# Kernel optimization log

Measured on AMD Instinct MI355X. Metric: run time of the kernel, lower is better.

The kernel has to match this reference:

```python
import jax, jax.numpy as jnp
import numpy as np

N = 100000      # nodes
E = 1600000     # edges
F_IN = 128
HID = 64
N_CLS = 40


def setup_inputs() -> dict:
    key = jax.random.key(0)
    ks = jax.random.split(key, 8)
    x = jax.random.normal(ks[0], (N, F_IN), dtype=jnp.float32)
    edge_index = jax.random.randint(ks[1], (2, E), 0, N, dtype=jnp.int64)
    # SAGEConv params: lin_l (applied to mean-aggregated neighbors, with bias),
    # lin_r (applied to root/self features, no bias). Glorot-ish init scaling.
    W1_l = jax.random.normal(ks[2], (F_IN, HID), dtype=jnp.float32) / np.sqrt(F_IN)
    b1 = jnp.zeros((HID,), dtype=jnp.float32)
    W1_r = jax.random.normal(ks[3], (F_IN, HID), dtype=jnp.float32) / np.sqrt(F_IN)
    W2_l = jax.random.normal(ks[4], (HID, N_CLS), dtype=jnp.float32) / np.sqrt(HID)
    b2 = jnp.zeros((N_CLS,), dtype=jnp.float32)
    W2_r = jax.random.normal(ks[5], (HID, N_CLS), dtype=jnp.float32) / np.sqrt(HID)
    return {"x": x, "edge_index": edge_index,
            "W1_l": W1_l, "b1": b1, "W1_r": W1_r,
            "W2_l": W2_l, "b2": b2, "W2_r": W2_r}


def _sage_conv(x, src, dst, W_l, b_l, W_r):
    # mean aggregation of neighbor features: messages flow src -> dst
    msgs = x[src]                                              # [E, d]
    summed = jax.ops.segment_sum(msgs, dst, num_segments=N)    # [N, d]
    cnt = jax.ops.segment_sum(jnp.ones((src.shape[0],), x.dtype), dst,
                              num_segments=N)                  # [N]
    agg = summed / jnp.maximum(cnt, 1.0)[:, None]
    return agg @ W_l + b_l + x @ W_r


def reference(x, edge_index, W1_l, b1, W1_r, W2_l, b2, W2_r):
    src, dst = edge_index[0], edge_index[1]
    h = jax.nn.relu(_sage_conv(x, src, dst, W1_l, b1, W1_r))
    # dropout: identity in eval mode
    logits = _sage_conv(h, src, dst, W2_l, b2, W2_r)
    return jax.nn.log_softmax(logits, axis=1)
```

## Files before the change

### kernel.cpp

```cpp
#include <hip/hip_runtime.h>
#include <math.h>

#define N_NODES 100000
#define F_IN    128
#define HID     64
#define N_CLS   40
#define MT      (N_NODES / 16)

#define BSHIFT  9
#define BSZ     512
#define NB      ((N_NODES + BSZ - 1) / BSZ)
#define EPB     4096

typedef __attribute__((ext_vector_type(8))) short bf8_t;
typedef __attribute__((ext_vector_type(4))) float f4_t;
typedef __attribute__((ext_vector_type(2))) float f2v_t;

typedef unsigned short ushort_t;
typedef unsigned int uint_t;
typedef unsigned char uchar_t;

__device__ __forceinline__ ushort_t f2b(float f) {
    union { float f; uint_t u; } c; c.f = f;
    uint_t u = c.u + 0x7FFFu + ((c.u >> 16) & 1u);
    return (ushort_t)(u >> 16);
}
__device__ __forceinline__ float b2f(ushort_t h) {
    union { uint_t u; float f; } c; c.u = ((uint_t)h) << 16;
    return c.f;
}

#if defined(__has_builtin)
#if __has_builtin(__builtin_amdgcn_cvt_pk_f32_fp8) && __has_builtin(__builtin_amdgcn_cvt_pk_fp8_f32)
#define HAVE_FP8_HW 1
#endif
#endif

__device__ __forceinline__ uchar_t fp8_enc(float v) {
#ifdef HAVE_FP8_HW
    return (uchar_t)(__builtin_amdgcn_cvt_pk_fp8_f32(v, v, 0, false) & 0xff);
#else
    union { float f; uint_t u; } c; c.f = v;
    uint_t s = c.u >> 31;
    float av = fabsf(v);
    if (av > 448.f) av = 448.f;
    int e;
    float m = frexpf(av, &e);
    int ee = e + 6;
    uchar_t r;
    if (av == 0.f) r = 0;
    else if (ee <= 0) {
        int q = (int)(av * 512.f + 0.5f);
        if (q > 7) q = 7;
        r = (uchar_t)q;
    } else {
        int q = (int)(m * 16.f + 0.5f);
        if (q == 16) { q = 8; ee += 1; }
        if (ee > 15) { ee = 15; q = 15; }
        r = (uchar_t)((ee << 3) | (q & 7));
    }
    return r | (uchar_t)(s << 7);
#endif
}

__device__ __forceinline__ f2v_t fp8x2_dec_lo(uint_t w) {
#ifdef HAVE_FP8_HW
    return __builtin_amdgcn_cvt_pk_f32_fp8(w, false);
#else
    f2v_t r;
    for (int k = 0; k < 2; ++k) {
        uchar_t b = (w >> (8 * k)) & 0xff;
        uint_t s = (b >> 7) & 1, e = (b >> 3) & 15, m = b & 7;
        float f;
        if (e) { union { uint_t u; float ff; } c;
                 c.u = (s << 31) | ((e + 120) << 23) | (m << 20); f = c.ff; }
        else   { f = (float)m * 0.001953125f; if (s) f = -f; }
        r[k] = f;
    }
    return r;
#endif
}
__device__ __forceinline__ f2v_t fp8x2_dec_hi(uint_t w) {
#ifdef HAVE_FP8_HW
    return __builtin_amdgcn_cvt_pk_f32_fp8(w, true);
#else
    return fp8x2_dec_lo(w >> 16);
#endif
}

__global__ void block_hist_kernel(const int* __restrict__ ei, int E,
                                  int* __restrict__ blockHist) {
    __shared__ int cnt[NB];
    int t = threadIdx.x, blk = blockIdx.x;
    for (int i = t; i < NB; i += 256) cnt[i] = 0;
    __syncthreads();
    int e0 = blk * EPB;
#pragma unroll
    for (int i = 0; i < EPB / 256; ++i) {
        int e = e0 + i * 256 + t;
        if (e < E) atomicAdd(&cnt[ei[E + e] >> BSHIFT], 1);
    }
    __syncthreads();
    for (int i = t; i < NB; i += 256) blockHist[blk * NB + i] = cnt[i];
}

__global__ void col_scan_kernel(const int* __restrict__ blockHist, int nblk,
                                int* __restrict__ blockBase,
                                int* __restrict__ btot) {
    __shared__ int ss[256];
    __shared__ int carry;
    int bin = blockIdx.x, t = threadIdx.x;
    if (t == 0) carry = 0;
    __syncthreads();
    for (int c0 = 0; c0 < nblk; c0 += 256) {
        int b = c0 + t;
        int v = (b < nblk) ? blockHist[b * NB + bin] : 0;
        ss[t] = v;
        __syncthreads();
        for (int off = 1; off < 256; off <<= 1) {
            int u = (t >= off) ? ss[t - off] : 0;
            __syncthreads();
            ss[t] += u;
            __syncthreads();
        }
        if (b < nblk) blockBase[b * NB + bin] = carry + ss[t] - v;
        __syncthreads();
        if (t == 255) carry += ss[255];
        __syncthreads();
    }
    if (t == 0) btot[bin] = carry;
}

__global__ void scatter_pairs_kernel(const int* __restrict__ ei, int E,
                                     const int* __restrict__ blockBase,
                                     const int* __restrict__ btot,
                                     uint_t* __restrict__ pairs) {
    __shared__ int cur[NB];
    __shared__ int base[NB];
    __shared__ int ss[256];
    int t = threadIdx.x, blk = blockIdx.x;
    int v = (t < NB) ? btot[t] : 0;
    ss[t] = v;
    __syncthreads();
    for (int off = 1; off < 256; off <<= 1) {
        int u = (t >= off) ? ss[t - off] : 0;
        __syncthreads();
        ss[t] += u;
        __syncthreads();
    }
    if (t < NB) {
        cur[t] = 0;
        base[t] = (ss[t] - v) + blockBase[blk * NB + t];
    }
    __syncthreads();
    int e0 = blk * EPB;
#pragma unroll
    for (int i = 0; i < EPB / 256; ++i) {
        int e = e0 + i * 256 + t;
        if (e < E) {
            int src = ei[e];
            int dst = ei[E + e];
            int bin = dst >> BSHIFT;
            int r = atomicAdd(&cur[bin], 1);
            pairs[base[bin] + r] = ((uint_t)src << BSHIFT) | (uint_t)(dst & (BSZ - 1));
        }
    }
}

__global__ void bucket_sort_kernel(const uint_t* __restrict__ pairs,
                                   const int* __restrict__ btot,
                                   int* __restrict__ rowptr,
                                   int* __restrict__ csr) {
    __shared__ int hist[BSZ];
    __shared__ int lofs[BSZ];
    int bin = blockIdx.x, t = threadIdx.x;
    int pv = (t < NB) ? btot[t] : 0;
    lofs[t] = pv;
    __syncthreads();
    for (int off = 1; off < BSZ; off <<= 1) {
        int u = (t >= off) ? lofs[t - off] : 0;
        __syncthreads();
        lofs[t] += u;
        __syncthreads();
    }
    int base = (bin > 0) ? lofs[bin - 1] : 0;
    int cnt = btot[bin];
    __syncthreads();
    hist[t] = 0;
    __syncthreads();
    for (int i = t; i < cnt; i += BSZ)
        atomicAdd(&hist[pairs[base + i] & (BSZ - 1)], 1);
    __syncthreads();
    int v = hist[t];
    lofs[t] = v;
    __syncthreads();
    for (int off = 1; off < BSZ; off <<= 1) {
        int u = (t >= off) ? lofs[t - off] : 0;
        __syncthreads();
        lofs[t] += u;
        __syncthreads();
    }
    int excl = lofs[t] - v;
    int d_global = (bin << BSHIFT) + t;
    if (d_global < N_NODES) rowptr[d_global] = base + excl;
    if (bin == NB - 1 && t == 0) rowptr[N_NODES] = base + cnt;
    __syncthreads();
    lofs[t] = excl;
    hist[t] = 0;
    __syncthreads();
    for (int i = t; i < cnt; i += BSZ) {
        uint_t p = pairs[base + i];
        int lb = p & (BSZ - 1);
        int r = atomicAdd(&hist[lb], 1);
        csr[base + lofs[lb] + r] = (int)(p >> BSHIFT);
    }
}

__global__ void cvt_w_kernel(const float* __restrict__ W1l,
                             const float* __restrict__ W1r,
                             const float* __restrict__ W2l,
                             const float* __restrict__ W2r,
                             ushort_t* __restrict__ W1t,
                             ushort_t* __restrict__ W2t) {
    int t = blockIdx.x * blockDim.x + threadIdx.x;
    if (t < 128 * F_IN) {
        int n = t / F_IN, k = t - n * F_IN;
        float v = (n < HID) ? W1l[k * HID + n] : W1r[k * HID + (n - HID)];
        W1t[t] = f2b(v);
    } else if (t < 128 * F_IN + 80 * HID) {
        int u = t - 128 * F_IN;
        int n = u / HID, k = u - n * HID;
        float v = (n < N_CLS) ? W2l[k * N_CLS + n] : W2r[k * N_CLS + (n - N_CLS)];
        W2t[u] = f2b(v);
    }
}

__global__ void gemm1_mfma_kernel(const float* __restrict__ x,
                                  const ushort_t* __restrict__ W1t,
                                  uchar_t* __restrict__ y1f8,
                                  ushort_t* __restrict__ z1b) {
    __shared__ uchar_t sy[128][80];
    __shared__ ushort_t sz[128][72];
    int tid = threadIdx.x;
    int wave = tid >> 6, lane = tid & 63;
    int tile0 = blockIdx.x * 8 + wave * 2;
    int m0b = blockIdx.x * 128;
    int r = lane & 15, q = lane >> 4;
    bool v0 = (tile0 < MT), v1 = (tile0 + 1 < MT);

    bf8_t a0[4], a1[4];
#pragma unroll
    for (int kt = 0; kt < 4; ++kt) { a0[kt] = (bf8_t)(short)0; a1[kt] = (bf8_t)(short)0; }
    if (v0) {
        const float* xr = x + (size_t)(tile0 * 16 + r) * F_IN + q * 8;
#pragma unroll
        for (int kt = 0; kt < 4; ++kt) {
            float4 u = *(const float4*)(xr + kt * 32);
            float4 v = *(const float4*)(xr + kt * 32 + 4);
            bf8_t tt;
            tt[0] = (short)f2b(u.x); tt[1] = (short)f2b(u.y);
            tt[2] = (short)f2b(u.z); tt[3] = (short)f2b(u.w);
            tt[4] = (short)f2b(v.x); tt[5] = (short)f2b(v.y);
            tt[6] = (short)f2b(v.z); tt[7] = (short)f2b(v.w);
            a0[kt] = tt;
        }
    }
    if (v1) {
        const float* xr = x + (size_t)((tile0 + 1) * 16 + r) * F_IN + q * 8;
#pragma unroll
        for (int kt = 0; kt < 4; ++kt) {
            float4 u = *(const float4*)(xr + kt * 32);
            float4 v = *(const float4*)(xr + kt * 32 + 4);
            bf8_t tt;
            tt[0] = (short)f2b(u.x); tt[1] = (short)f2b(u.y);
            tt[2] = (short)f2b(u.z); tt[3] = (short)f2b(u.w);
            tt[4] = (short)f2b(v.x); tt[5] = (short)f2b(v.y);
            tt[6] = (short)f2b(v.z); tt[7] = (short)f2b(v.w);
            a1[kt] = tt;
        }
    }
    int lr0 = wave * 32 + q * 4;
#pragma unroll
    for (int tn = 0; tn < 8; ++tn) {
        const ushort_t* wr = W1t + (size_t)(tn * 16 + r) * F_IN + q * 8;
        bf8_t b[4];
#pragma unroll
        for (int kt = 0; kt < 4; ++kt)
            b[kt] = *(const bf8_t*)(wr + kt * 32);
        f4_t acc0 = {0.f, 0.f, 0.f, 0.f};
        f4_t acc1 = {0.f, 0.f, 0.f, 0.f};
#pragma unroll
        for (int kt = 0; kt < 4; ++kt) {
            acc0 = __builtin_amdgcn_mfma_f32_16x16x32_bf16(a0[kt], b[kt], acc0, 0, 0, 0);
            acc1 = __builtin_amdgcn_mfma_f32_16x16x32_bf16(a1[kt], b[kt], acc1, 0, 0, 0);
        }
        int col = tn * 16 + r;
        if (col < 64) {
            if (v0) {
#pragma unroll
                for (int rr = 0; rr < 4; ++rr) sy[lr0 + rr][col] = fp8_enc(acc0[rr]);
            }
            if (v1) {
#pragma unroll
                for (int rr = 0; rr < 4; ++rr) sy[lr0 + 16 + rr][col] = fp8_enc(acc1[rr]);
            }
        } else {
            if (v0) {
#pragma unroll
                for (int rr = 0; rr < 4; ++rr) sz[lr0 + rr][col - 64] = f2b(acc0[rr]);
            }
            if (v1) {
#pragma unroll
                for (int rr = 0; rr < 4; ++rr) sz[lr0 + 16 + rr][col - 64] = f2b(acc1[rr]);
            }
        }
    }
    __syncthreads();
    int vrows = N_NODES - m0b; if (vrows > 128) vrows = 128;
    for (int idx = tid; idx < vrows * 4; idx += 256) {
        int row = idx >> 2, c = (idx & 3) << 4;
        *(uint4*)(y1f8 + (size_t)(m0b + row) * 64 + c) = *(const uint4*)&sy[row][c];
    }
    for (int idx = tid; idx < vrows * 8; idx += 256) {
        int row = idx >> 3, c = (idx & 7) << 3;
        *(uint4*)(z1b + (size_t)(m0b + row) * HID + c) = *(const uint4*)&sz[row][c];
    }
}

__device__ __forceinline__ void acc16(float* acc, uint4 v) {
    f2v_t p;
    p = fp8x2_dec_lo(v.x); acc[0]  += p[0]; acc[1]  += p[1];
    p = fp8x2_dec_hi(v.x); acc[2]  += p[0]; acc[3]  += p[1];
    p = fp8x2_dec_lo(v.y); acc[4]  += p[0]; acc[5]  += p[1];
    p = fp8x2_dec_hi(v.y); acc[6]  += p[0]; acc[7]  += p[1];
    p = fp8x2_dec_lo(v.z); acc[8]  += p[0]; acc[9]  += p[1];
    p = fp8x2_dec_hi(v.z); acc[10] += p[0]; acc[11] += p[1];
    p = fp8x2_dec_lo(v.w); acc[12] += p[0]; acc[13] += p[1];
    p = fp8x2_dec_hi(v.w); acc[14] += p[0]; acc[15] += p[1];
}

__global__ void agg1_kernel(const int* __restrict__ rowptr,
                            const int* __restrict__ csr,
                            const uchar_t* __restrict__ y1f8,
                            const ushort_t* __restrict__ z1b,
                            const float* __restrict__ b1,
                            ushort_t* __restrict__ hb,
                            uchar_t* __restrict__ hf8) {
    int gid = blockIdx.x * blockDim.x + threadIdx.x;
    int wave = gid >> 6, lane = gid & 63;
    int g = lane >> 2, l = lane & 3;
    int n = wave * 16 + g;
    if (n >= N_NODES) return;
    int beg = rowptr[n], end = rowptr[n + 1];
    float acc[16];
#pragma unroll
    for (int j = 0; j < 16; ++j) acc[j] = 0.f;
    const uchar_t* yb = y1f8 + l * 16;
    int i = beg;
    for (; i + 3 < end; i += 4) {
        int s0 = csr[i], s1 = csr[i + 1], s2 = csr[i + 2], s3 = csr[i + 3];
        uint4 w0 = *(const uint4*)(yb + (size_t)s0 * 64);
        uint4 w1 = *(const uint4*)(yb + (size_t)s1 * 64);
        uint4 w2 = *(const uint4*)(yb + (size_t)s2 * 64);
        uint4 w3 = *(const uint4*)(yb + (size_t)s3 * 64);
        acc16(acc, w0); acc16(acc, w1); acc16(acc, w2); acc16(acc, w3);
    }
    for (; i < end; ++i) {
        uint4 w = *(const uint4*)(yb + (size_t)csr[i] * 64);
        acc16(acc, w);
    }
    float inv = 1.0f / fmaxf((float)(end - beg), 1.0f);
    int c = l * 16;
    ushort_t zz[16];
    *(uint4*)&zz[0] = *(const uint4*)(z1b + (size_t)n * HID + c);
    *(uint4*)&zz[8] = *(const uint4*)(z1b + (size_t)n * HID + c + 8);
    float bv[16];
    *(float4*)&bv[0]  = *(const float4*)(b1 + c);
    *(float4*)&bv[4]  = *(const float4*)(b1 + c + 4);
    *(float4*)&bv[8]  = *(const float4*)(b1 + c + 8);
    *(float4*)&bv[12] = *(const float4*)(b1 + c + 12);
    ushort_t o[16];
    uchar_t of[16];
#pragma unroll
    for (int j = 0; j < 16; ++j) {
        float r = fmaxf(fmaf(acc[j], inv, bv[j] + b2f(zz[j])), 0.f);
        o[j] = f2b(r);
        of[j] = fp8_enc(r);
    }
    *(uint4*)(hb + (size_t)n * HID + c)     = *(const uint4*)&o[0];
    *(uint4*)(hb + (size_t)n * HID + c + 8) = *(const uint4*)&o[8];
    *(uint4*)(hf8 + (size_t)n * 64 + c)     = *(const uint4*)&of[0];
}

__global__ void agg2m_kernel(const int* __restrict__ rowptr,
                             const int* __restrict__ csr,
                             const uchar_t* __restrict__ hf8,
                             ushort_t* __restrict__ mb) {
    int gid = blockIdx.x * blockDim.x + threadIdx.x;
    int wave = gid >> 6, lane = gid & 63;
    int g = lane >> 2, l = lane & 3;
    int n = wave * 16 + g;
    if (n >= N_NODES) return;
    int beg = rowptr[n], end = rowptr[n + 1];
    float acc[16];
#pragma unroll
    for (int j = 0; j < 16; ++j) acc[j] = 0.f;
    const uchar_t* yb = hf8 + l * 16;
    int i = beg;
    for (; i + 3 < end; i += 4) {
        int s0 = csr[i], s1 = csr[i + 1], s2 = csr[i + 2], s3 = csr[i + 3];
        uint4 w0 = *(const uint4*)(yb + (size_t)s0 * 64);
        uint4 w1 = *(const uint4*)(yb + (size_t)s1 * 64);
        uint4 w2 = *(const uint4*)(yb + (size_t)s2 * 64);
        uint4 w3 = *(const uint4*)(yb + (size_t)s3 * 64);
        acc16(acc, w0); acc16(acc, w1); acc16(acc, w2); acc16(acc, w3);
    }
    for (; i < end; ++i) {
        uint4 w = *(const uint4*)(yb + (size_t)csr[i] * 64);
        acc16(acc, w);
    }
    float inv = 1.0f / fmaxf((float)(end - beg), 1.0f);
    int c = l * 16;
    ushort_t o[16];
#pragma unroll
    for (int j = 0; j < 16; ++j)
        o[j] = f2b(acc[j] * inv);
    *(uint4*)(mb + (size_t)n * HID + c)     = *(const uint4*)&o[0];
    *(uint4*)(mb + (size_t)n * HID + c + 8) = *(const uint4*)&o[8];
}

__global__ void gemm2_fused_kernel(const ushort_t* __restrict__ mb,
                                   const ushort_t* __restrict__ hb,
                                   const ushort_t* __restrict__ W2t,
                                   const float* __restrict__ b2,
                                   float* __restrict__ out) {
    __shared__ float sOut[64][44];
    int tid = threadIdx.x;
    int wave = tid >> 6, lane = tid & 63;
    int tile = blockIdx.x * 4 + wave;
    int m0b = blockIdx.x * 64;
    if (tile < MT) {
        int m0 = tile * 16;
        int r = lane & 15, q = lane >> 4;
        const ushort_t* mr = mb + (size_t)(m0 + r) * HID + q * 8;
        const ushort_t* hr = hb + (size_t)(m0 + r) * HID + q * 8;
        bf8_t a0[2], a1[2];
#pragma unroll
        for (int kt = 0; kt < 2; ++kt) {
            a0[kt] = *(const bf8_t*)(mr + kt * 32);
            a1[kt] = *(const bf8_t*)(hr + kt * 32);
        }
        float v[3][4];
#pragma unroll
        for (int tn = 0; tn < 3; ++tn) {
            int col = tn * 16 + r;
            int cl = (col < N_CLS) ? col : 0;
            const ushort_t* wl = W2t + (size_t)cl * HID + q * 8;
            const ushort_t* wrp = W2t + (size_t)(N_CLS + cl) * HID + q * 8;
            f4_t acc = {0.f, 0.f, 0.f, 0.f};
#pragma unroll
            for (int kt = 0; kt < 2; ++kt) {
                bf8_t bl = *(const bf8_t*)(wl + kt * 32);
                acc = __builtin_amdgcn_mfma_f32_16x16x32_bf16(a0[kt], bl, acc, 0, 0, 0);
            }
#pragma unroll
            for (int kt = 0; kt < 2; ++kt) {
                bf8_t br = *(const bf8_t*)(wrp + kt * 32);
                acc = __builtin_amdgcn_mfma_f32_16x16x32_bf16(a1[kt], br, acc, 0, 0, 0);
            }
            float bias = (col < N_CLS) ? b2[cl] : 0.f;
#pragma unroll
            for (int rr = 0; rr < 4; ++rr)
                v[tn][rr] = (col < N_CLS) ? (acc[rr] + bias) : -INFINITY;
        }
        int lrow = wave * 16 + q * 4;
#pragma unroll
        for (int rr = 0; rr < 4; ++rr) {
            float m = fmaxf(fmaxf(v[0][rr], v[1][rr]), v[2][rr]);
#pragma unroll
            for (int off = 1; off < 16; off <<= 1)
                m = fmaxf(m, __shfl_xor(m, off, 64));
            float s = 0.f;
#pragma unroll
            for (int tn = 0; tn < 3; ++tn)
                if (v[tn][rr] > -INFINITY) s += expf(v[tn][rr] - m);
#pragma unroll
            for (int off = 1; off < 16; off <<= 1)
                s += __shfl_xor(s, off, 64);
            float ls = m + logf(s);
#pragma unroll
            for (int tn = 0; tn < 3; ++tn) {
                int col = tn * 16 + r;
                if (col < N_CLS)
                    sOut[lrow + rr][col] = v[tn][rr] - ls;
            }
        }
    }
    __syncthreads();
    int vrows = N_NODES - m0b; if (vrows > 64) vrows = 64;
    for (int idx = tid; idx < vrows * 10; idx += 256) {
        int row = idx / 10, c = (idx - row * 10) * 4;
        *(float4*)(out + (size_t)(m0b + row) * N_CLS + c) = *(const float4*)&sOut[row][c];
    }
}

extern "C" void kernel_launch(void* const* d_in, const int* in_sizes, int n_in,
                              void* d_out, int out_size, void* d_ws, size_t ws_size,
                              hipStream_t stream) {
    const float* x   = (const float*)d_in[0];
    const int*   ei  = (const int*)d_in[1];
    const float* W1l = (const float*)d_in[2];
    const float* b1  = (const float*)d_in[3];
    const float* W1r = (const float*)d_in[4];
    const float* W2l = (const float*)d_in[5];
    const float* b2  = (const float*)d_in[6];
    const float* W2r = (const float*)d_in[7];
    float* out = (float*)d_out;
    const int E = in_sizes[1] / 2;
    const int nblk = (E + EPB - 1) / EPB;

    char* p = (char*)d_ws;
    auto take = [&](size_t bytes) {
        char* q = p;
        p += (bytes + 15) & ~(size_t)15;
        return (void*)q;
    };
    int* rowptr     = (int*)take(sizeof(int) * (N_NODES + 4));
    int* blockHist  = (int*)take(sizeof(int) * (size_t)nblk * NB);
    int* blockBase  = (int*)take(sizeof(int) * (size_t)nblk * NB);
    int* btot       = (int*)take(sizeof(int) * NB);
    uint_t* pairs   = (uint_t*)take(sizeof(uint_t) * (size_t)E);
    int* csr        = (int*)take(sizeof(int) * (size_t)E);
    ushort_t* W1t   = (ushort_t*)take(sizeof(ushort_t) * 128 * F_IN);
    ushort_t* W2t   = (ushort_t*)take(sizeof(ushort_t) * 80 * HID);
    uchar_t* y1f8   = (uchar_t*)take(sizeof(uchar_t) * (size_t)N_NODES * 64);
    ushort_t* z1b   = (ushort_t*)take(sizeof(ushort_t) * (size_t)N_NODES * HID);
    ushort_t* hb    = (ushort_t*)take(sizeof(ushort_t) * (size_t)N_NODES * HID);
    uchar_t* hf8    = (uchar_t*)take(sizeof(uchar_t) * (size_t)N_NODES * 64);
    ushort_t* mb    = (ushort_t*)take(sizeof(ushort_t) * (size_t)N_NODES * HID);

    const int B = 256;

    block_hist_kernel<<<nblk, 256, 0, stream>>>(ei, E, blockHist);
    col_scan_kernel<<<NB, 256, 0, stream>>>(blockHist, nblk, blockBase, btot);
    scatter_pairs_kernel<<<nblk, 256, 0, stream>>>(ei, E, blockBase, btot, pairs);
    bucket_sort_kernel<<<NB, BSZ, 0, stream>>>(pairs, btot, rowptr, csr);

    cvt_w_kernel<<<(128 * F_IN + 80 * HID + B - 1) / B, B, 0, stream>>>(
        W1l, W1r, W2l, W2r, W1t, W2t);

    int gemm1_blocks = (MT + 7) / 8;
    int gemm2_blocks = (MT + 3) / 4;
    int t_agg = (N_NODES / 16) * 64;

    gemm1_mfma_kernel<<<gemm1_blocks, B, 0, stream>>>(x, W1t, y1f8, z1b);
    agg1_kernel<<<(t_agg + B - 1) / B, B, 0, stream>>>(rowptr, csr, y1f8, z1b, b1, hb, hf8);
    agg2m_kernel<<<(t_agg + B - 1) / B, B, 0, stream>>>(rowptr, csr, hf8, mb);
    gemm2_fused_kernel<<<gemm2_blocks, B, 0, stream>>>(mb, hb, W2t, b2, out);
}
```

Before: 232.1 us.

## Replace multi-pass edge bucketing with atomic arena scatter; fuse layer-2 aggregation into GEMM

The CSR build changes from a histogram, column scan and scatter pipeline into one scatter pass. Each block reserves space in fixed-capacity per-bucket arenas through global atomics, and the gcur reset is folded into the weight conversion kernel. Layer-2 mean aggregation now writes its bf16 results to shared memory and feeds the MFMA GEMM and log-softmax in the same kernel, so the intermediate mb buffer and its round trip are gone. This drops three launches, but the arena assumes no bucket exceeds CAP edges, which holds only for roughly uniform degree distributions. Edge order within a bucket also becomes nondeterministic, which can change the floating-point summation order.

```diff
diff --git a/kernel.cpp b/kernel.cpp
--- a/kernel.cpp
+++ b/kernel.cpp
@@ -11,6 +11,7 @@
 #define BSZ     512
 #define NB      ((N_NODES + BSZ - 1) / BSZ)
 #define EPB     4096
+#define CAP     9216
 
 typedef __attribute__((ext_vector_type(8))) short bf8_t;
 typedef __attribute__((ext_vector_type(4))) float f4_t;
@@ -88,141 +89,15 @@
 #endif
 }
 
-__global__ void block_hist_kernel(const int* __restrict__ ei, int E,
-                                  int* __restrict__ blockHist) {
-    __shared__ int cnt[NB];
-    int t = threadIdx.x, blk = blockIdx.x;
-    for (int i = t; i < NB; i += 256) cnt[i] = 0;
-    __syncthreads();
-    int e0 = blk * EPB;
-#pragma unroll
-    for (int i = 0; i < EPB / 256; ++i) {
-        int e = e0 + i * 256 + t;
-        if (e < E) atomicAdd(&cnt[ei[E + e] >> BSHIFT], 1);
-    }
-    __syncthreads();
-    for (int i = t; i < NB; i += 256) blockHist[blk * NB + i] = cnt[i];
-}
-
-__global__ void col_scan_kernel(const int* __restrict__ blockHist, int nblk,
-                                int* __restrict__ blockBase,
-                                int* __restrict__ btot) {
-    __shared__ int ss[256];
-    __shared__ int carry;
-    int bin = blockIdx.x, t = threadIdx.x;
-    if (t == 0) carry = 0;
-    __syncthreads();
-    for (int c0 = 0; c0 < nblk; c0 += 256) {
-        int b = c0 + t;
-        int v = (b < nblk) ? blockHist[b * NB + bin] : 0;
-        ss[t] = v;
-        __syncthreads();
-        for (int off = 1; off < 256; off <<= 1) {
-            int u = (t >= off) ? ss[t - off] : 0;
-            __syncthreads();
-            ss[t] += u;
-            __syncthreads();
-        }
-        if (b < nblk) blockBase[b * NB + bin] = carry + ss[t] - v;
-        __syncthreads();
-        if (t == 255) carry += ss[255];
-        __syncthreads();
-    }
-    if (t == 0) btot[bin] = carry;
-}
-
-__global__ void scatter_pairs_kernel(const int* __restrict__ ei, int E,
-                                     const int* __restrict__ blockBase,
-                                     const int* __restrict__ btot,
-                                     uint_t* __restrict__ pairs) {
-    __shared__ int cur[NB];
-    __shared__ int base[NB];
-    __shared__ int ss[256];
-    int t = threadIdx.x, blk = blockIdx.x;
-    int v = (t < NB) ? btot[t] : 0;
-    ss[t] = v;
-    __syncthreads();
-    for (int off = 1; off < 256; off <<= 1) {
-        int u = (t >= off) ? ss[t - off] : 0;
-        __syncthreads();
-        ss[t] += u;
-        __syncthreads();
-    }
-    if (t < NB) {
-        cur[t] = 0;
-        base[t] = (ss[t] - v) + blockBase[blk * NB + t];
-    }
-    __syncthreads();
-    int e0 = blk * EPB;
-#pragma unroll
-    for (int i = 0; i < EPB / 256; ++i) {
-        int e = e0 + i * 256 + t;
-        if (e < E) {
-            int src = ei[e];
-            int dst = ei[E + e];
-            int bin = dst >> BSHIFT;
-            int r = atomicAdd(&cur[bin], 1);
-            pairs[base[bin] + r] = ((uint_t)src << BSHIFT) | (uint_t)(dst & (BSZ - 1));
-        }
-    }
-}
-
-__global__ void bucket_sort_kernel(const uint_t* __restrict__ pairs,
-                                   const int* __restrict__ btot,
-                                   int* __restrict__ rowptr,
-                                   int* __restrict__ csr) {
-    __shared__ int hist[BSZ];
-    __shared__ int lofs[BSZ];
-    int bin = blockIdx.x, t = threadIdx.x;
-    int pv = (t < NB) ? btot[t] : 0;
-    lofs[t] = pv;
-    __syncthreads();
-    for (int off = 1; off < BSZ; off <<= 1) {
-        int u = (t >= off) ? lofs[t - off] : 0;
-        __syncthreads();
-        lofs[t] += u;
-        __syncthreads();
-    }
-    int base = (bin > 0) ? lofs[bin - 1] : 0;
-    int cnt = btot[bin];
-    __syncthreads();
-    hist[t] = 0;
-    __syncthreads();
-    for (int i = t; i < cnt; i += BSZ)
-        atomicAdd(&hist[pairs[base + i] & (BSZ - 1)], 1);
-    __syncthreads();
-    int v = hist[t];
-    lofs[t] = v;
-    __syncthreads();
-    for (int off = 1; off < BSZ; off <<= 1) {
-        int u = (t >= off) ? lofs[t - off] : 0;
-        __syncthreads();
-        lofs[t] += u;
-        __syncthreads();
-    }
-    int excl = lofs[t] - v;
-    int d_global = (bin << BSHIFT) + t;
-    if (d_global < N_NODES) rowptr[d_global] = base + excl;
-    if (bin == NB - 1 && t == 0) rowptr[N_NODES] = base + cnt;
-    __syncthreads();
-    lofs[t] = excl;
-    hist[t] = 0;
-    __syncthreads();
-    for (int i = t; i < cnt; i += BSZ) {
-        uint_t p = pairs[base + i];
-        int lb = p & (BSZ - 1);
-        int r = atomicAdd(&hist[lb], 1);
-        csr[base + lofs[lb] + r] = (int)(p >> BSHIFT);
-    }
-}
-
-__global__ void cvt_w_kernel(const float* __restrict__ W1l,
-                             const float* __restrict__ W1r,
-                             const float* __restrict__ W2l,
-                             const float* __restrict__ W2r,
-                             ushort_t* __restrict__ W1t,
-                             ushort_t* __restrict__ W2t) {
+__global__ void init_cvt_kernel(const float* __restrict__ W1l,
+                                const float* __restrict__ W1r,
+                                const float* __restrict__ W2l,
+                                const float* __restrict__ W2r,
+                                ushort_t* __restrict__ W1t,
+                                ushort_t* __restrict__ W2t,
+                                int* __restrict__ gcur) {
     int t = blockIdx.x * blockDim.x + threadIdx.x;
+    if (t < NB) gcur[t] = 0;
     if (t < 128 * F_IN) {
         int n = t / F_IN, k = t - n * F_IN;
         float v = (n < HID) ? W1l[k * HID + n] : W1r[k * HID + (n - HID)];
@@ -232,6 +107,91 @@
         int n = u / HID, k = u - n * HID;
         float v = (n < N_CLS) ? W2l[k * N_CLS + n] : W2r[k * N_CLS + (n - N_CLS)];
         W2t[u] = f2b(v);
+    }
+}
+
+__global__ void scatter_direct_kernel(const int* __restrict__ ei, int E,
+                                      int* __restrict__ gcur,
+                                      uint_t* __restrict__ arena) {
+    __shared__ int cnt[NB];
+    __shared__ int rbase[NB];
+    __shared__ int cur[NB];
+    int t = threadIdx.x, blk = blockIdx.x;
+    for (int i = t; i < NB; i += 256) { cnt[i] = 0; cur[i] = 0; }
+    __syncthreads();
+    int e0 = blk * EPB;
+#pragma unroll
+    for (int i = 0; i < EPB / 256; ++i) {
+        int e = e0 + i * 256 + t;
+        if (e < E) atomicAdd(&cnt[ei[E + e] >> BSHIFT], 1);
+    }
+    __syncthreads();
+    for (int i = t; i < NB; i += 256) {
+        int c = cnt[i];
+        rbase[i] = c ? atomicAdd(&gcur[i], c) : 0;
+    }
+    __syncthreads();
+#pragma unroll
+    for (int i = 0; i < EPB / 256; ++i) {
+        int e = e0 + i * 256 + t;
+        if (e < E) {
+            int src = ei[e];
+            int dst = ei[E + e];
+            int bin = dst >> BSHIFT;
+            int r = atomicAdd(&cur[bin], 1);
+            arena[(size_t)bin * CAP + rbase[bin] + r] =
+                ((uint_t)src << BSHIFT) | (uint_t)(dst & (BSZ - 1));
+        }
+    }
+}
+
+__global__ void bucket_sort_kernel(const uint_t* __restrict__ arena,
+                                   const int* __restrict__ gcur,
+                                   int* __restrict__ rowptr,
+                                   int* __restrict__ csr) {
+    __shared__ int hist[BSZ];
+    __shared__ int lofs[BSZ];
+    int bin = blockIdx.x, t = threadIdx.x;
+    int pv = (t < NB) ? gcur[t] : 0;
+    lofs[t] = pv;
+    __syncthreads();
+    for (int off = 1; off < BSZ; off <<= 1) {
+        int u = (t >= off) ? lofs[t - off] : 0;
+        __syncthreads();
+        lofs[t] += u;
+        __syncthreads();
+    }
+    int base = (bin > 0) ? lofs[bin - 1] : 0;
+    int cnt = gcur[bin];
+    __syncthreads();
+    hist[t] = 0;
+    __syncthreads();
+    const uint_t* ap = arena + (size_t)bin * CAP;
+    for (int i = t; i < cnt; i += BSZ)
+        atomicAdd(&hist[ap[i] & (BSZ - 1)], 1);
+    __syncthreads();
+    int v = hist[t];
+    lofs[t] = v;
+    __syncthreads();
+    for (int off = 1; off < BSZ; off <<= 1) {
+        int u = (t >= off) ? lofs[t - off] : 0;
+        __syncthreads();
+        lofs[t] += u;
+        __syncthreads();
+    }
+    int excl = lofs[t] - v;
+    int d_global = (bin << BSHIFT) + t;
+    if (d_global < N_NODES) rowptr[d_global] = base + excl;
+    if (bin == NB - 1 && t == 0) rowptr[N_NODES] = base + cnt;
+    __syncthreads();
+    lofs[t] = excl;
+    hist[t] = 0;
+    __syncthreads();
+    for (int i = t; i < cnt; i += BSZ) {
+        uint_t p = ap[i];
+        int lb = p & (BSZ - 1);
+        int r = atomicAdd(&hist[lb], 1);
+        csr[base + lofs[lb] + r] = (int)(p >> BSHIFT);
     }
 }
 
@@ -392,62 +352,60 @@
     *(uint4*)(hf8 + (size_t)n * 64 + c)     = *(const uint4*)&of[0];
 }
 
-__global__ void agg2m_kernel(const int* __restrict__ rowptr,
-                             const int* __restrict__ csr,
-                             const uchar_t* __restrict__ hf8,
-                             ushort_t* __restrict__ mb) {
-    int gid = blockIdx.x * blockDim.x + threadIdx.x;
-    int wave = gid >> 6, lane = gid & 63;
-    int g = lane >> 2, l = lane & 3;
-    int n = wave * 16 + g;
-    if (n >= N_NODES) return;
-    int beg = rowptr[n], end = rowptr[n + 1];
-    float acc[16];
-#pragma unroll
-    for (int j = 0; j < 16; ++j) acc[j] = 0.f;
-    const uchar_t* yb = hf8 + l * 16;
-    int i = beg;
-    for (; i + 3 < end; i += 4) {
-        int s0 = csr[i], s1 = csr[i + 1], s2 = csr[i + 2], s3 = csr[i + 3];
-        uint4 w0 = *(const uint4*)(yb + (size_t)s0 * 64);
-        uint4 w1 = *(const uint4*)(yb + (size_t)s1 * 64);
-        uint4 w2 = *(const uint4*)(yb + (size_t)s2 * 64);
-        uint4 w3 = *(const uint4*)(yb + (size_t)s3 * 64);
-        acc16(acc, w0); acc16(acc, w1); acc16(acc, w2); acc16(acc, w3);
-    }
-    for (; i < end; ++i) {
-        uint4 w = *(const uint4*)(yb + (size_t)csr[i] * 64);
-        acc16(acc, w);
-    }
-    float inv = 1.0f / fmaxf((float)(end - beg), 1.0f);
-    int c = l * 16;
-    ushort_t o[16];
-#pragma unroll
-    for (int j = 0; j < 16; ++j)
-        o[j] = f2b(acc[j] * inv);
-    *(uint4*)(mb + (size_t)n * HID + c)     = *(const uint4*)&o[0];
-    *(uint4*)(mb + (size_t)n * HID + c + 8) = *(const uint4*)&o[8];
-}
-
-__global__ void gemm2_fused_kernel(const ushort_t* __restrict__ mb,
-                                   const ushort_t* __restrict__ hb,
-                                   const ushort_t* __restrict__ W2t,
-                                   const float* __restrict__ b2,
-                                   float* __restrict__ out) {
-    __shared__ float sOut[64][44];
+__global__ void layer2_fused_kernel(const int* __restrict__ rowptr,
+                                    const int* __restrict__ csr,
+                                    const uchar_t* __restrict__ hf8,
+                                    const ushort_t* __restrict__ hb,
+                                    const ushort_t* __restrict__ W2t,
+                                    const float* __restrict__ b2,
+                                    float* __restrict__ out) {
+    __shared__ ushort_t sA[64][72];
+    __shared__ float sO[64][44];
     int tid = threadIdx.x;
     int wave = tid >> 6, lane = tid & 63;
-    int tile = blockIdx.x * 4 + wave;
     int m0b = blockIdx.x * 64;
-    if (tile < MT) {
-        int m0 = tile * 16;
+    int tileN = m0b + wave * 16;
+    bool valid = (tileN < N_NODES);
+
+    if (valid) {
+        int g = lane >> 2, l = lane & 3;
+        int n = tileN + g;
+        int beg = rowptr[n], end = rowptr[n + 1];
+        float acc[16];
+#pragma unroll
+        for (int j = 0; j < 16; ++j) acc[j] = 0.f;
+        const uchar_t* yb = hf8 + l * 16;
+        int i = beg;
+        for (; i + 3 < end; i += 4) {
+            int s0 = csr[i], s1 = csr[i + 1], s2 = csr[i + 2], s3 = csr[i + 3];
+            uint4 w0 = *(const uint4*)(yb + (size_t)s0 * 64);
+            uint4 w1 = *(const uint4*)(yb + (size_t)s1 * 64);
+            uint4 w2 = *(const uint4*)(yb + (size_t)s2 * 64);
+            uint4 w3 = *(const uint4*)(yb + (size_t)s3 * 64);
+            acc16(acc, w0); acc16(acc, w1); acc16(acc, w2); acc16(acc, w3);
+        }
+        for (; i < end; ++i) {
+            uint4 w = *(const uint4*)(yb + (size_t)csr[i] * 64);
+            acc16(acc, w);
+        }
+        float inv = 1.0f / fmaxf((float)(end - beg), 1.0f);
+        ushort_t o[16];
+#pragma unroll
+        for (int j = 0; j < 16; ++j)
+            o[j] = f2b(acc[j] * inv);
+        int lrow = wave * 16 + g;
+        *(uint4*)&sA[lrow][l * 16]     = *(const uint4*)&o[0];
+        *(uint4*)&sA[lrow][l * 16 + 8] = *(const uint4*)&o[8];
+    }
+    __syncthreads();
+    if (valid) {
         int r = lane & 15, q = lane >> 4;
-        const ushort_t* mr = mb + (size_t)(m0 + r) * HID + q * 8;
-        const ushort_t* hr = hb + (size_t)(m0 + r) * HID + q * 8;
+        const ushort_t* ar = &sA[wave * 16 + r][q * 8];
+        const ushort_t* hr = hb + (size_t)(tileN + r) * HID + q * 8;
         bf8_t a0[2], a1[2];
 #pragma unroll
         for (int kt = 0; kt < 2; ++kt) {
-            a0[kt] = *(const bf8_t*)(mr + kt * 32);
+            a0[kt] = *(const bf8_t*)(ar + kt * 32);
             a1[kt] = *(const bf8_t*)(hr + kt * 32);
         }
         float v[3][4];
@@ -455,23 +413,23 @@
         for (int tn = 0; tn < 3; ++tn) {
             int col = tn * 16 + r;
             int cl = (col < N_CLS) ? col : 0;
-            const ushort_t* wl = W2t + (size_t)cl * HID + q * 8;
-            const ushort_t* wrp = W2t + (size_t)(N_CLS + cl) * HID + q * 8;
-            f4_t acc = {0.f, 0.f, 0.f, 0.f};
+            const ushort_t* wl  = W2t + (size_t)cl * HID + q * 8;
+            const ushort_t* wr2 = W2t + (size_t)(N_CLS + cl) * HID + q * 8;
+            f4_t acc4 = {0.f, 0.f, 0.f, 0.f};
 #pragma unroll
             for (int kt = 0; kt < 2; ++kt) {
                 bf8_t bl = *(const bf8_t*)(wl + kt * 32);
-                acc = __builtin_amdgcn_mfma_f32_16x16x32_bf16(a0[kt], bl, acc, 0, 0, 0);
+                acc4 = __builtin_amdgcn_mfma_f32_16x16x32_bf16(a0[kt], bl, acc4, 0, 0, 0);
             }
 #pragma unroll
             for (int kt = 0; kt < 2; ++kt) {
-                bf8_t br = *(const bf8_t*)(wrp + kt * 32);
-                acc = __builtin_amdgcn_mfma_f32_16x16x32_bf16(a1[kt], br, acc, 0, 0, 0);
+                bf8_t br = *(const bf8_t*)(wr2 + kt * 32);
+                acc4 = __builtin_amdgcn_mfma_f32_16x16x32_bf16(a1[kt], br, acc4, 0, 0, 0);
             }
             float bias = (col < N_CLS) ? b2[cl] : 0.f;
 #pragma unroll
             for (int rr = 0; rr < 4; ++rr)
-                v[tn][rr] = (col < N_CLS) ? (acc[rr] + bias) : -INFINITY;
+                v[tn][rr] = (col < N_CLS) ? (acc4[rr] + bias) : -INFINITY;
         }
         int lrow = wave * 16 + q * 4;
 #pragma unroll
@@ -492,7 +450,7 @@
             for (int tn = 0; tn < 3; ++tn) {
                 int col = tn * 16 + r;
                 if (col < N_CLS)
-                    sOut[lrow + rr][col] = v[tn][rr] - ls;
+                    sO[lrow + rr][col] = v[tn][rr] - ls;
             }
         }
     }
@@ -500,7 +458,7 @@
     int vrows = N_NODES - m0b; if (vrows > 64) vrows = 64;
     for (int idx = tid; idx < vrows * 10; idx += 256) {
         int row = idx / 10, c = (idx - row * 10) * 4;
-        *(float4*)(out + (size_t)(m0b + row) * N_CLS + c) = *(const float4*)&sOut[row][c];
+        *(float4*)(out + (size_t)(m0b + row) * N_CLS + c) = *(const float4*)&sO[row][c];
     }
 }
 
@@ -526,10 +484,8 @@
         return (void*)q;
     };
     int* rowptr     = (int*)take(sizeof(int) * (N_NODES + 4));
-    int* blockHist  = (int*)take(sizeof(int) * (size_t)nblk * NB);
-    int* blockBase  = (int*)take(sizeof(int) * (size_t)nblk * NB);
-    int* btot       = (int*)take(sizeof(int) * NB);
-    uint_t* pairs   = (uint_t*)take(sizeof(uint_t) * (size_t)E);
+    int* gcur       = (int*)take(sizeof(int) * NB);
+    uint_t* arena   = (uint_t*)take(sizeof(uint_t) * (size_t)NB * CAP);
     int* csr        = (int*)take(sizeof(int) * (size_t)E);
     ushort_t* W1t   = (ushort_t*)take(sizeof(ushort_t) * 128 * F_IN);
     ushort_t* W2t   = (ushort_t*)take(sizeof(ushort_t) * 80 * HID);
@@ -537,24 +493,19 @@
     ushort_t* z1b   = (ushort_t*)take(sizeof(ushort_t) * (size_t)N_NODES * HID);
     ushort_t* hb    = (ushort_t*)take(sizeof(ushort_t) * (size_t)N_NODES * HID);
     uchar_t* hf8    = (uchar_t*)take(sizeof(uchar_t) * (size_t)N_NODES * 64);
-    ushort_t* mb    = (ushort_t*)take(sizeof(ushort_t) * (size_t)N_NODES * HID);
 
     const int B = 256;
 
-    block_hist_kernel<<<nblk, 256, 0, stream>>>(ei, E, blockHist);
-    col_scan_kernel<<<NB, 256, 0, stream>>>(blockHist, nblk, blockBase, btot);
-    scatter_pairs_kernel<<<nblk, 256, 0, stream>>>(ei, E, blockBase, btot, pairs);
-    bucket_sort_kernel<<<NB, BSZ, 0, stream>>>(pairs, btot, rowptr, csr);
-
-    cvt_w_kernel<<<(128 * F_IN + 80 * HID + B - 1) / B, B, 0, stream>>>(
-        W1l, W1r, W2l, W2r, W1t, W2t);
+    init_cvt_kernel<<<(128 * F_IN + 80 * HID + B - 1) / B, B, 0, stream>>>(
+        W1l, W1r, W2l, W2r, W1t, W2t, gcur);
+    scatter_direct_kernel<<<nblk, 256, 0, stream>>>(ei, E, gcur, arena);
+    bucket_sort_kernel<<<NB, BSZ, 0, stream>>>(arena, gcur, rowptr, csr);
 
     int gemm1_blocks = (MT + 7) / 8;
-    int gemm2_blocks = (MT + 3) / 4;
+    int l2_blocks = (N_NODES + 63) / 64;
     int t_agg = (N_NODES / 16) * 64;
 
     gemm1_mfma_kernel<<<gemm1_blocks, B, 0, stream>>>(x, W1t, y1f8, z1b);
     agg1_kernel<<<(t_agg + B - 1) / B, B, 0, stream>>>(rowptr, csr, y1f8, z1b, b1, hb, hf8);
-    agg2m_kernel<<<(t_agg + B - 1) / B, B, 0, stream>>>(rowptr, csr, hf8, mb);
-    gemm2_fused_kernel<<<gemm2_blocks, B, 0, stream>>>(mb, hb, W2t, b2, out);
-}
+    layer2_fused_kernel<<<l2_blocks, B, 0, stream>>>(rowptr, csr, hf8, hb, W2t, b2, out);
+}
```

After: 244.0 us. 5.1% more time.
